# Kernel tuning notes

Hardware: AMD Instinct MI355X
Metric: run time of the kernel (lower is better)

## Reference

```python
import jax, jax.numpy as jnp
import numpy as np

B, L, E, H = 4, 1024, 2048, 16
DH = E // H
SCALE_BASE = 512.0


def _rotate_every_two(x):
    x1 = x[..., ::2]
    x2 = x[..., 1::2]
    return jnp.stack([-x2, x1], axis=-1).reshape(x.shape)


def _xpos(x, downscale):
    # x: [BH, L, Dh]; non-incremental path => offset = 0
    length = x.shape[1]
    head_dim = x.shape[-1]
    min_pos = -(length // 2)
    positions = jnp.arange(min_pos, length + min_pos, dtype=jnp.float32)  # [L]
    base = (jnp.arange(0, head_dim, 2, dtype=jnp.float32) + 0.4 * head_dim) / (1.4 * head_dim)  # [Dh/2]
    scale = base[None, :] ** (positions[:, None] / SCALE_BASE)  # [L, Dh/2]
    # fixed_pos_embedding over `scale` (seq_len=L, dim=Dh/2), positions 0..L-1
    dim = head_dim // 2
    inv_freq = 1.0 / (10000.0 ** (jnp.arange(0, dim, dtype=jnp.float32) / dim))
    sinusoid = jnp.arange(length, dtype=jnp.float32)[:, None] * inv_freq[None, :]
    sin, cos = jnp.sin(sinusoid), jnp.cos(sinusoid)
    if downscale:
        scale = 1.0 / scale
    sin_s = jnp.repeat(sin * scale, 2, axis=-1)  # duplicate_interleave -> [L, Dh]
    cos_s = jnp.repeat(cos * scale, 2, axis=-1)
    return x * cos_s + _rotate_every_two(x) * sin_s


def setup_inputs() -> dict:
    key = jax.random.key(0)
    ks = jax.random.split(key, 6)
    w_std = 1.0 / np.sqrt(E)
    query = jax.random.normal(ks[0], (B, L, E), dtype=jnp.float32)
    Wq = jax.random.normal(ks[1], (E, E), dtype=jnp.float32) * w_std
    Wk = jax.random.normal(ks[2], (E, E), dtype=jnp.float32) * w_std
    Wv = jax.random.normal(ks[3], (E, E), dtype=jnp.float32) * w_std
    Wo = jax.random.normal(ks[4], (E, E), dtype=jnp.float32) * w_std
    bq = jnp.zeros((E,), jnp.float32)
    bk = jnp.zeros((E,), jnp.float32)
    bv = jnp.zeros((E,), jnp.float32)
    bo = jnp.zeros((E,), jnp.float32)
    # causal additive mask [L, L]: 0 on/below diag, large negative above
    attn_mask = jnp.where(jnp.triu(jnp.ones((L, L), bool), k=1), -1e9, 0.0).astype(jnp.float32)
    rel_pos = jax.random.normal(ks[5], (B * H, L, L), dtype=jnp.float32) * 0.02
    return {"query": query, "Wq": Wq, "bq": bq, "Wk": Wk, "bk": bk, "Wv": Wv,
            "bv": bv, "Wo": Wo, "bo": bo, "attn_mask": attn_mask, "rel_pos": rel_pos}


def reference(query, Wq, bq, Wk, bk, Wv, bv, Wo, bo, attn_mask, rel_pos):
    scaling = DH ** -0.5
    q = (query @ Wq.T + bq) * scaling
    k = query @ Wk.T + bk
    v = query @ Wv.T + bv

    def split(t):  # [B, L, E] -> [B*H, L, Dh]
        return t.reshape(B, L, H, DH).transpose(0, 2, 1, 3).reshape(B * H, L, DH)

    q, k, v = split(q), split(k), split(v)
    k = _xpos(k, downscale=True)
    q = _xpos(q, downscale=False)

    w = jnp.einsum('btd,bsd->bts', q, k)          # [B*H, L, L]
    w = jnp.nan_to_num(w) + attn_mask[None]
    w = w + rel_pos
    w = jax.nn.softmax(w.astype(jnp.float32), axis=-1).astype(w.dtype)
    attn = jnp.einsum('bts,bsd->btd', w, v)       # [B*H, L, Dh]
    attn = attn.reshape(B, H, L, DH).transpose(0, 2, 1, 3).reshape(B, L, E)
    out = attn @ Wo.T + bo
    attn_weights = w.reshape(B, H, L, L).transpose(1, 0, 2, 3)  # [H, B, L, L]
    return out, attn_weights
```

## Files before the change

kernel.cpp:

```cpp
#include <hip/hip_runtime.h>
#include <math.h>

#define BB 4
#define LL 1024
#define EE 2048
#define HH 16
#define DHD 128
#define NTOK 4096
#define NBH 64
#define OUT0_ELEMS 8388608

typedef __attribute__((ext_vector_type(8))) short short8;
typedef __attribute__((ext_vector_type(4))) float f32x4;
typedef __attribute__((ext_vector_type(4))) unsigned short ushort4v;
typedef __attribute__((ext_vector_type(8))) unsigned short ushort8v;

__device__ __forceinline__ unsigned short f2bf(float x) {
    union { float f; unsigned int u; } v; v.f = x;
    unsigned int r = v.u + 0x7FFFu + ((v.u >> 16) & 1u);
    return (unsigned short)(r >> 16);
}
__device__ __forceinline__ float bf2f(unsigned short h) {
    union { unsigned int u; float f; } v; v.u = ((unsigned int)h) << 16;
    return v.f;
}

__device__ __forceinline__ void gload16(const void* g, void* l) {
    __builtin_amdgcn_global_load_lds((const __attribute__((address_space(1))) void*)g,
                                     (__attribute__((address_space(3))) void*)l,
                                     16, 0, 0);
}

__global__ __launch_bounds__(256) void cvt_k(const float* __restrict__ in,
                                             unsigned short* __restrict__ out, int n) {
    int i = (blockIdx.x * 256 + threadIdx.x) * 8;
    if (i >= n) return;
    float4 a = *(const float4*)(in + i);
    float4 b = *(const float4*)(in + i + 4);
    ushort4v u, w;
    u.x = f2bf(a.x); u.y = f2bf(a.y); u.z = f2bf(a.z); u.w = f2bf(a.w);
    w.x = f2bf(b.x); w.y = f2bf(b.y); w.z = f2bf(b.z); w.w = f2bf(b.w);
    *(ushort4v*)(out + i) = u;
    *(ushort4v*)(out + i + 4) = w;
}

__global__ __launch_bounds__(64) void xpos_table_k(float4* __restrict__ tab) {
    int t = blockIdx.x;
    int j = threadIdx.x;
    float pos = (float)(t - 512);
    float base = (2.0f * (float)j + 51.2f) * (1.0f / 179.2f);
    float sc = powf(base, pos * (1.0f / 512.0f));
    float inv_freq = powf(10000.0f, -(float)j * (1.0f / 64.0f));
    float ang = (float)t * inv_freq;
    float s = sinf(ang);
    float c = cosf(ang);
    tab[(t << 6) | j] = make_float4(c * sc, s * sc, c / sc, s / sc);
}

__global__ __launch_bounds__(256) void xpos_apply_k(unsigned short* __restrict__ q,
                                                    unsigned short* __restrict__ k,
                                                    const float4* __restrict__ tab) {
    int g = blockIdx.x * 256 + threadIdx.x;
    int jj = g & 15;
    int t = (g >> 4) & 1023;
    int bh = g >> 14;
    size_t off = (((size_t)((bh << 10) | t)) << 7) + jj * 8;
    ushort8v qv = *(const ushort8v*)(q + off);
    ushort8v kv = *(const ushort8v*)(k + off);
    ushort8v qo, ko;
#pragma unroll
    for (int p = 0; p < 4; ++p) {
        float4 tb = tab[(t << 6) | (jj * 4 + p)];
        float qx = bf2f(qv[2 * p]), qy = bf2f(qv[2 * p + 1]);
        float kx = bf2f(kv[2 * p]), ky = bf2f(kv[2 * p + 1]);
        qo[2 * p]     = f2bf(qx * tb.x - qy * tb.y);
        qo[2 * p + 1] = f2bf(qy * tb.x + qx * tb.y);
        ko[2 * p]     = f2bf(kx * tb.z - ky * tb.w);
        ko[2 * p + 1] = f2bf(ky * tb.z + kx * tb.w);
    }
    *(ushort8v*)(q + off) = qo;
    *(ushort8v*)(k + off) = ko;
}

__global__ __launch_bounds__(256)
void mmqkv_k(const unsigned short* __restrict__ Abf, const unsigned short* __restrict__ Wqkv,
             const float* __restrict__ bq, const float* __restrict__ bk,
             const float* __restrict__ bv, unsigned short* __restrict__ qb,
             unsigned short* __restrict__ kb, unsigned short* __restrict__ vt,
             float scaling) {
    __shared__ alignas(16) unsigned short lA[128 * 32];
    __shared__ alignas(16) unsigned short lB[128 * 32];

    const int tid = threadIdx.x;
    const int lane = tid & 63;
    const int wave = tid >> 6;
    const int wr = wave >> 1, wc = wave & 1;
    const int fr = lane & 15, fq = lane >> 4;
    const int m0 = blockIdx.y * 128, n0 = blockIdx.x * 128;
    const int w = n0 >> 11;
    const float* bsel = (w == 0) ? bq : (w == 1) ? bk : bv;
    const float alpha = (w == 0) ? scaling : 1.0f;

    f32x4 acc[4][4];
#pragma unroll
    for (int i = 0; i < 4; ++i)
#pragma unroll
        for (int j = 0; j < 4; ++j) acc[i][j] = (f32x4){0.f, 0.f, 0.f, 0.f};

    for (int k0 = 0; k0 < 2048; k0 += 32) {
#pragma unroll
        for (int i = 0; i < 2; ++i) {
            int c = i * 256 + tid;
            int r = c >> 2, kc = c & 3;
            gload16(Abf + (size_t)(m0 + r) * 2048 + k0 + kc * 8, &lA[c * 8]);
        }
#pragma unroll
        for (int i = 0; i < 2; ++i) {
            int c = i * 256 + tid;
            int r = c >> 2, kc = c & 3;
            gload16(Wqkv + (size_t)(n0 + r) * 2048 + k0 + kc * 8, &lB[c * 8]);
        }
        __syncthreads();

        short8 afr[4], bfr[4];
#pragma unroll
        for (int mi = 0; mi < 4; ++mi)
            afr[mi] = *(const short8*)&lA[(wr * 64 + mi * 16 + fr) * 32 + fq * 8];
#pragma unroll
        for (int ni = 0; ni < 4; ++ni)
            bfr[ni] = *(const short8*)&lB[(wc * 64 + ni * 16 + fr) * 32 + fq * 8];
#pragma unroll
        for (int mi = 0; mi < 4; ++mi)
#pragma unroll
            for (int ni = 0; ni < 4; ++ni)
                acc[mi][ni] = __builtin_amdgcn_mfma_f32_16x16x32_bf16(
                    afr[mi], bfr[ni], acc[mi][ni], 0, 0, 0);
        __syncthreads();
    }

#pragma unroll
    for (int mi = 0; mi < 4; ++mi) {
#pragma unroll
        for (int ni = 0; ni < 4; ++ni) {
#pragma unroll
            for (int r = 0; r < 4; ++r) {
                int m = m0 + wr * 64 + mi * 16 + fq * 4 + r;
                int n = n0 + wc * 64 + ni * 16 + fr;
                int nn = n & 2047;
                int b_ = m >> 10, t = m & 1023, h = nn >> 7, d = nn & 127;
                float v = alpha * (acc[mi][ni][r] + bsel[nn]);
                if (w == 0)
                    qb[(((size_t)(b_ * HH + h) << 10 | t) << 7) | d] = f2bf(v);
                else if (w == 1)
                    kb[(((size_t)(b_ * HH + h) << 10 | t) << 7) | d] = f2bf(v);
                else
                    vt[((size_t)((b_ * HH + h) * 128 + d) << 10) | t] = f2bf(v);
            }
        }
    }
}

__global__ __launch_bounds__(256)
void mmo_k(const unsigned short* __restrict__ Abf, const unsigned short* __restrict__ Bp,
           const float* __restrict__ bias, float* __restrict__ C) {
    __shared__ alignas(16) unsigned short lA[128 * 32];
    __shared__ alignas(16) unsigned short lB[128 * 32];

    const int tid = threadIdx.x;
    const int lane = tid & 63;
    const int wave = tid >> 6;
    const int wr = wave >> 1, wc = wave & 1;
    const int fr = lane & 15, fq = lane >> 4;
    const int m0 = blockIdx.y * 128, n0 = blockIdx.x * 128;

    f32x4 acc[4][4];
#pragma unroll
    for (int i = 0; i < 4; ++i)
#pragma unroll
        for (int j = 0; j < 4; ++j) acc[i][j] = (f32x4){0.f, 0.f, 0.f, 0.f};

    for (int k0 = 0; k0 < 2048; k0 += 32) {
#pragma unroll
        for (int i = 0; i < 2; ++i) {
            int c = i * 256 + tid;
            int r = c >> 2, kc = c & 3;
            gload16(Abf + (size_t)(m0 + r) * 2048 + k0 + kc * 8, &lA[c * 8]);
        }
#pragma unroll
        for (int i = 0; i < 2; ++i) {
            int c = i * 256 + tid;
            int r = c >> 2, kc = c & 3;
            gload16(Bp + (size_t)(n0 + r) * 2048 + k0 + kc * 8, &lB[c * 8]);
        }
        __syncthreads();

        short8 afr[4], bfr[4];
#pragma unroll
        for (int mi = 0; mi < 4; ++mi)
            afr[mi] = *(const short8*)&lA[(wr * 64 + mi * 16 + fr) * 32 + fq * 8];
#pragma unroll
        for (int ni = 0; ni < 4; ++ni)
            bfr[ni] = *(const short8*)&lB[(wc * 64 + ni * 16 + fr) * 32 + fq * 8];
#pragma unroll
        for (int mi = 0; mi < 4; ++mi)
#pragma unroll
            for (int ni = 0; ni < 4; ++ni)
                acc[mi][ni] = __builtin_amdgcn_mfma_f32_16x16x32_bf16(
                    afr[mi], bfr[ni], acc[mi][ni], 0, 0, 0);
        __syncthreads();
    }

#pragma unroll
    for (int mi = 0; mi < 4; ++mi)
#pragma unroll
        for (int ni = 0; ni < 4; ++ni)
#pragma unroll
            for (int r = 0; r < 4; ++r) {
                int m = m0 + wr * 64 + mi * 16 + fq * 4 + r;
                int n = n0 + wc * 64 + ni * 16 + fr;
                C[(size_t)m * EE + n] = acc[mi][ni][r] + bias[n];
            }
}

__global__ __launch_bounds__(256)
void scores_k(const unsigned short* __restrict__ qb, const unsigned short* __restrict__ kb,
              const float* __restrict__ rel, unsigned short* __restrict__ ebuf,
              float* __restrict__ psum) {
    __shared__ alignas(16) char smem[16384];
    unsigned short* lA = (unsigned short*)smem;
    unsigned short* lB = (unsigned short*)(smem + 8192);
    float* slab = (float*)smem;

    const int tid = threadIdx.x;
    const int lane = tid & 63, wave = tid >> 6;
    const int wr = wave >> 1, wc = wave & 1;
    const int fr = lane & 15, fq = lane >> 4;

    int idx = blockIdx.x;
    int tt = (int)((sqrtf(8.f * (float)idx + 1.f) - 1.f) * 0.5f);
    while ((tt + 1) * (tt + 2) / 2 <= idx) ++tt;
    while (tt * (tt + 1) / 2 > idx) --tt;
    const int ss = idx - tt * (tt + 1) / 2;
    const int t0 = tt << 7, s0 = ss << 7;
    const int bh = blockIdx.y;

    const unsigned short* Q = qb + ((size_t)bh << 17);
    const unsigned short* K = kb + ((size_t)bh << 17);

    f32x4 acc[4][4];
#pragma unroll
    for (int i = 0; i < 4; ++i)
#pragma unroll
        for (int j = 0; j < 4; ++j) acc[i][j] = (f32x4){0.f, 0.f, 0.f, 0.f};

    for (int k0 = 0; k0 < 128; k0 += 32) {
#pragma unroll
        for (int i = 0; i < 2; ++i) {
            int c = i * 256 + tid;
            int r = c >> 2, kc = c & 3;
            gload16(Q + (size_t)(t0 + r) * 128 + k0 + kc * 8, &lA[c * 8]);
        }
#pragma unroll
        for (int i = 0; i < 2; ++i) {
            int c = i * 256 + tid;
            int r = c >> 2, kc = c & 3;
            gload16(K + (size_t)(s0 + r) * 128 + k0 + kc * 8, &lB[c * 8]);
        }
        __syncthreads();

        short8 afr[4], bfr[4];
#pragma unroll
        for (int mi = 0; mi < 4; ++mi)
            afr[mi] = *(const short8*)&lA[(wr * 64 + mi * 16 + fr) * 32 + fq * 8];
#pragma unroll
        for (int ni = 0; ni < 4; ++ni)
            bfr[ni] = *(const short8*)&lB[(wc * 64 + ni * 16 + fr) * 32 + fq * 8];
#pragma unroll
        for (int mi = 0; mi < 4; ++mi)
#pragma unroll
            for (int ni = 0; ni < 4; ++ni)
                acc[mi][ni] = __builtin_amdgcn_mfma_f32_16x16x32_bf16(
                    afr[mi], bfr[ni], acc[mi][ni], 0, 0, 0);
        __syncthreads();
    }

    unsigned short* EO = ebuf + ((size_t)bh << 20);
    const float* RLb = rel + ((size_t)bh << 20);
#pragma unroll
    for (int sl = 0; sl < 4; ++sl) {
        if (wr == (sl >> 1)) {
#pragma unroll
            for (int mi2 = 0; mi2 < 2; ++mi2) {
                int mi = ((sl & 1) << 1) + mi2;
#pragma unroll
                for (int ni = 0; ni < 4; ++ni)
#pragma unroll
                    for (int r = 0; r < 4; ++r) {
                        int srow = (mi2 << 4) + (fq << 2) + r;
                        int col = (wc << 6) + (ni << 4) + fr;
                        slab[srow * 128 + (col ^ (((srow >> 2) & 3) << 4))] = acc[mi][ni][r];
                    }
            }
        }
        __syncthreads();
        {
            int srow = tid >> 3;
            int tg = t0 + (sl << 5) + srow;
            const float* RL = RLb + ((size_t)tg << 10) + s0;
            unsigned short* ER = EO + ((size_t)tg << 10) + s0;
            float rsum = 0.f;
#pragma unroll
            for (int c = 0; c < 4; ++c) {
                int col = ((tid & 7) << 2) + (c << 5);
                float4 sv = *(const float4*)&slab[srow * 128 + (col ^ (((srow >> 2) & 3) << 4))];
                float4 rl = *(const float4*)(RL + col);
                float4 e;
                e.x = (s0 + col     <= tg) ? __expf(sv.x + rl.x - 15.f) : 0.f;
                e.y = (s0 + col + 1 <= tg) ? __expf(sv.y + rl.y - 15.f) : 0.f;
                e.z = (s0 + col + 2 <= tg) ? __expf(sv.z + rl.z - 15.f) : 0.f;
                e.w = (s0 + col + 3 <= tg) ? __expf(sv.w + rl.w - 15.f) : 0.f;
                ushort4v h;
                h.x = f2bf(e.x); h.y = f2bf(e.y); h.z = f2bf(e.z); h.w = f2bf(e.w);
                *(ushort4v*)(ER + col) = h;
                rsum += e.x + e.y + e.z + e.w;
            }
            rsum += __shfl_xor(rsum, 1);
            rsum += __shfl_xor(rsum, 2);
            rsum += __shfl_xor(rsum, 4);
            if ((tid & 7) == 0)
                psum[((((size_t)bh << 10) + tg) << 3) + ss] = rsum;
        }
        __syncthreads();
    }
}

__global__ __launch_bounds__(256)
void pvw_k(const unsigned short* __restrict__ ebuf, const unsigned short* __restrict__ vt,
           const float* __restrict__ psum, float* __restrict__ attnP,
           unsigned short* __restrict__ am) {
    __shared__ alignas(16) unsigned short lE[64 * 64];
    __shared__ alignas(16) unsigned short lV[128 * 64];
    __shared__ float lInvF[64];

    const int tid = threadIdx.x;
    const int lane = tid & 63, wave = tid >> 6;
    const int wr = wave >> 1, wc = wave & 1;
    const int fr = lane & 15, fq = lane >> 4;
    const int strip = 15 - blockIdx.x;
    const int t0 = strip << 6;
    const int bh = blockIdx.y;
    const int hh = bh & 15, bb = bh >> 4;
    const int n_s = (t0 >> 6) + 1;

    const unsigned short* EB = ebuf + ((size_t)bh << 20) + ((size_t)t0 << 10);
    const unsigned short* Vb = vt + ((size_t)bh << 17);
    float* PO = attnP + (((size_t)(hh * BB + bb)) << 20) + ((size_t)t0 << 10);

    if (tid < 64) {
        const float* p = psum + ((((size_t)bh << 10) + t0 + tid) << 3);
        const int tt = t0 >> 7;
        float s = 0.f;
#pragma unroll
        for (int j = 0; j < 8; ++j) s += (j <= tt) ? p[j] : 0.f;
        lInvF[tid] = 1.f / s;
    }
    __syncthreads();

    f32x4 acc[2][4];
#pragma unroll
    for (int i = 0; i < 2; ++i)
#pragma unroll
        for (int j = 0; j < 4; ++j) acc[i][j] = (f32x4){0.f, 0.f, 0.f, 0.f};

    for (int j = 0; j < n_s; ++j) {
        int s0 = j << 6;
#pragma unroll
        for (int i = 0; i < 2; ++i) {
            int o = (i * 256 + tid) * 16;
            int r = o >> 7;
            int cb = (o & 127) ^ ((r & 7) << 4);
            gload16(EB + (size_t)r * 1024 + s0 + (cb >> 1), (char*)lE + o);
        }
#pragma unroll
        for (int i = 0; i < 4; ++i) {
            int o = (i * 256 + tid) * 16;
            int r = o >> 7;
            int cb = (o & 127) ^ ((r & 7) << 4);
            gload16(Vb + (size_t)r * 1024 + s0 + (cb >> 1), (char*)lV + o);
        }
        __syncthreads();

        {
            int row = tid >> 2, col0 = (tid & 3) << 4;
            float inv = lInvF[row];
            float* PR = PO + (size_t)row * 1024 + s0 + col0;
#pragma unroll
            for (int cc = 0; cc < 2; ++cc) {
                int cbyte = ((col0 + cc * 8) * 2) ^ ((row & 7) << 4);
                ushort8v ev = *(const ushort8v*)((const char*)lE + row * 128 + cbyte);
                float4 p0, p1;
                p0.x = bf2f(ev[0]) * inv; p0.y = bf2f(ev[1]) * inv;
                p0.z = bf2f(ev[2]) * inv; p0.w = bf2f(ev[3]) * inv;
                p1.x = bf2f(ev[4]) * inv; p1.y = bf2f(ev[5]) * inv;
                p1.z = bf2f(ev[6]) * inv; p1.w = bf2f(ev[7]) * inv;
                *(float4*)(PR + cc * 8) = p0;
                *(float4*)(PR + cc * 8 + 4) = p1;
            }
        }

#pragma unroll
        for (int ks = 0; ks < 2; ++ks) {
            short8 pf[2], vf[4];
#pragma unroll
            for (int mi = 0; mi < 2; ++mi) {
                int row = wr * 32 + mi * 16 + fr;
                int cb = (ks * 64 + fq * 16) ^ ((row & 7) << 4);
                pf[mi] = *(const short8*)((const char*)lE + row * 128 + cb);
            }
#pragma unroll
            for (int ni = 0; ni < 4; ++ni) {
                int row = wc * 64 + ni * 16 + fr;
                int cb = (ks * 64 + fq * 16) ^ ((row & 7) << 4);
                vf[ni] = *(const short8*)((const char*)lV + row * 128 + cb);
            }
#pragma unroll
            for (int mi = 0; mi < 2; ++mi)
#pragma unroll
                for (int ni = 0; ni < 4; ++ni)
                    acc[mi][ni] = __builtin_amdgcn_mfma_f32_16x16x32_bf16(
                        pf[mi], vf[ni], acc[mi][ni], 0, 0, 0);
        }
        __syncthreads();
    }

    {
        int row = tid >> 2;
        float4 z = make_float4(0.f, 0.f, 0.f, 0.f);
        for (int c = (n_s << 6) + ((tid & 3) << 2); c < 1024; c += 16)
            *(float4*)(PO + (size_t)row * 1024 + c) = z;
    }

#pragma unroll
    for (int mi = 0; mi < 2; ++mi)
#pragma unroll
        for (int ni = 0; ni < 4; ++ni)
#pragma unroll
            for (int r = 0; r < 4; ++r) {
                int tl = wr * 32 + mi * 16 + fq * 4 + r;
                int d = wc * 64 + ni * 16 + fr;
                float o = acc[mi][ni][r] * lInvF[tl];
                am[(((size_t)(bb * 1024 + t0 + tl)) << 11) + hh * 128 + d] = f2bf(o);
            }
}

extern "C" void kernel_launch(void* const* d_in, const int* in_sizes, int n_in,
                              void* d_out, int out_size, void* d_ws, size_t ws_size,
                              hipStream_t stream) {
    const float* query = (const float*)d_in[0];
    const float* Wq    = (const float*)d_in[1];
    const float* bq    = (const float*)d_in[2];
    const float* Wk    = (const float*)d_in[3];
    const float* bk    = (const float*)d_in[4];
    const float* Wv    = (const float*)d_in[5];
    const float* bv    = (const float*)d_in[6];
    const float* Wo    = (const float*)d_in[7];
    const float* bo    = (const float*)d_in[8];
    const float* rel   = (const float*)d_in[10];

    float* out    = (float*)d_out;
    float* attn_w = out + OUT0_ELEMS;

    char* w = (char*)d_ws;
    unsigned short* Xbf   = (unsigned short*)(w);
    unsigned short* Wqkvb = (unsigned short*)(w + (16 << 20));
    unsigned short* Wob   = (unsigned short*)(w + (40 << 20));
    unsigned short* qb    = (unsigned short*)(w + (48 << 20));
    unsigned short* kb    = (unsigned short*)(w + (64 << 20));
    unsigned short* vt    = (unsigned short*)(w + (80 << 20));
    unsigned short* am    = (unsigned short*)(w + (96 << 20));
    float4* tab           = (float4*)(w + (112 << 20));
    float* psum           = (float*)(w + (113u << 20));
    unsigned short* ebuf  = (unsigned short*)(w + (128u << 20));

    const float scaling = 0.08838834764831845f;

    xpos_table_k<<<LL, 64, 0, stream>>>(tab);

    cvt_k<<<4096, 256, 0, stream>>>(query, Xbf, OUT0_ELEMS);
    cvt_k<<<2048, 256, 0, stream>>>(Wq, Wqkvb, EE * EE);
    cvt_k<<<2048, 256, 0, stream>>>(Wk, Wqkvb + (size_t)EE * EE, EE * EE);
    cvt_k<<<2048, 256, 0, stream>>>(Wv, Wqkvb + 2 * (size_t)EE * EE, EE * EE);
    cvt_k<<<2048, 256, 0, stream>>>(Wo, Wob, EE * EE);

    dim3 gqkv(3 * EE / 128, NTOK / 128);
    mmqkv_k<<<gqkv, 256, 0, stream>>>(Xbf, Wqkvb, bq, bk, bv, qb, kb, vt, scaling);

    xpos_apply_k<<<(NBH * LL * 16) / 256, 256, 0, stream>>>(qb, kb, tab);

    dim3 gsc(36, NBH);
    scores_k<<<gsc, 256, 0, stream>>>(qb, kb, rel, ebuf, psum);

    dim3 gpv(16, NBH);
    pvw_k<<<gpv, 256, 0, stream>>>(ebuf, vt, psum, attn_w, am);

    dim3 gout(EE / 128, NTOK / 128);
    mmo_k<<<gout, 256, 0, stream>>>(am, Wob, bo, out);
}
```

Measured before the change: 481.5 us.

## Fuse weight conversions, fold xPos into QKV epilogue, reorder PV grid

The five fp32-to-bf16 conversion launches are merged into one kernel that indexes into the right source and destination. The xPos rotation is moved into the QKV GEMM epilogue: each lane gets its partner element with a lane shuffle and reads the sin/cos table, which removes the separate read-modify-write pass over q and k. The PV kernel grid is transposed so that blocks for heavy causal strips across all heads are scheduled first. The trade-off is extra table loads and shuffles in the GEMM epilogue.

After: 472.0 us. -2.0%, faster.

```diff
diff --git a/kernel.cpp b/kernel.cpp
--- a/kernel.cpp
+++ b/kernel.cpp
@@ -31,17 +31,31 @@
                                      16, 0, 0);
 }
 
-__global__ __launch_bounds__(256) void cvt_k(const float* __restrict__ in,
-                                             unsigned short* __restrict__ out, int n) {
-    int i = (blockIdx.x * 256 + threadIdx.x) * 8;
-    if (i >= n) return;
-    float4 a = *(const float4*)(in + i);
-    float4 b = *(const float4*)(in + i + 4);
+__global__ __launch_bounds__(256)
+void cvt_all_k(const float* __restrict__ X, const float* __restrict__ Wq,
+               const float* __restrict__ Wk, const float* __restrict__ Wv,
+               const float* __restrict__ Wo, unsigned short* __restrict__ Xbf,
+               unsigned short* __restrict__ Wqkvb, unsigned short* __restrict__ Wob) {
+    size_t g = (size_t)(blockIdx.x * 256 + threadIdx.x) * 8;
+    if (g >= 25165824u) return;
+    const float* src;
+    unsigned short* dst;
+    if (g < 8388608u) {
+        src = X + g; dst = Xbf + g;
+    } else {
+        size_t rr = g - 8388608u;
+        int wi = (int)(rr >> 22);
+        size_t o = rr & 4194303u;
+        src = (wi == 0 ? Wq : wi == 1 ? Wk : wi == 2 ? Wv : Wo) + o;
+        dst = (wi < 3 ? Wqkvb + ((size_t)wi << 22) : Wob) + o;
+    }
+    float4 a = *(const float4*)(src);
+    float4 b = *(const float4*)(src + 4);
     ushort4v u, w;
     u.x = f2bf(a.x); u.y = f2bf(a.y); u.z = f2bf(a.z); u.w = f2bf(a.w);
     w.x = f2bf(b.x); w.y = f2bf(b.y); w.z = f2bf(b.z); w.w = f2bf(b.w);
-    *(ushort4v*)(out + i) = u;
-    *(ushort4v*)(out + i + 4) = w;
+    *(ushort4v*)(dst) = u;
+    *(ushort4v*)(dst + 4) = w;
 }
 
 __global__ __launch_bounds__(64) void xpos_table_k(float4* __restrict__ tab) {
@@ -57,37 +71,12 @@
     tab[(t << 6) | j] = make_float4(c * sc, s * sc, c / sc, s / sc);
 }
 
-__global__ __launch_bounds__(256) void xpos_apply_k(unsigned short* __restrict__ q,
-                                                    unsigned short* __restrict__ k,
-                                                    const float4* __restrict__ tab) {
-    int g = blockIdx.x * 256 + threadIdx.x;
-    int jj = g & 15;
-    int t = (g >> 4) & 1023;
-    int bh = g >> 14;
-    size_t off = (((size_t)((bh << 10) | t)) << 7) + jj * 8;
-    ushort8v qv = *(const ushort8v*)(q + off);
-    ushort8v kv = *(const ushort8v*)(k + off);
-    ushort8v qo, ko;
-#pragma unroll
-    for (int p = 0; p < 4; ++p) {
-        float4 tb = tab[(t << 6) | (jj * 4 + p)];
-        float qx = bf2f(qv[2 * p]), qy = bf2f(qv[2 * p + 1]);
-        float kx = bf2f(kv[2 * p]), ky = bf2f(kv[2 * p + 1]);
-        qo[2 * p]     = f2bf(qx * tb.x - qy * tb.y);
-        qo[2 * p + 1] = f2bf(qy * tb.x + qx * tb.y);
-        ko[2 * p]     = f2bf(kx * tb.z - ky * tb.w);
-        ko[2 * p + 1] = f2bf(ky * tb.z + kx * tb.w);
-    }
-    *(ushort8v*)(q + off) = qo;
-    *(ushort8v*)(k + off) = ko;
-}
-
 __global__ __launch_bounds__(256)
 void mmqkv_k(const unsigned short* __restrict__ Abf, const unsigned short* __restrict__ Wqkv,
              const float* __restrict__ bq, const float* __restrict__ bk,
              const float* __restrict__ bv, unsigned short* __restrict__ qb,
              unsigned short* __restrict__ kb, unsigned short* __restrict__ vt,
-             float scaling) {
+             const float4* __restrict__ tab, float scaling) {
     __shared__ alignas(16) unsigned short lA[128 * 32];
     __shared__ alignas(16) unsigned short lB[128 * 32];
 
@@ -142,19 +131,26 @@
     for (int mi = 0; mi < 4; ++mi) {
 #pragma unroll
         for (int ni = 0; ni < 4; ++ni) {
+            int n = n0 + wc * 64 + ni * 16 + fr;
+            int nn = n & 2047;
+            int h = nn >> 7, d = nn & 127;
+            float bias = bsel[nn];
 #pragma unroll
             for (int r = 0; r < 4; ++r) {
                 int m = m0 + wr * 64 + mi * 16 + fq * 4 + r;
-                int n = n0 + wc * 64 + ni * 16 + fr;
-                int nn = n & 2047;
-                int b_ = m >> 10, t = m & 1023, h = nn >> 7, d = nn & 127;
-                float v = alpha * (acc[mi][ni][r] + bsel[nn]);
-                if (w == 0)
-                    qb[(((size_t)(b_ * HH + h) << 10 | t) << 7) | d] = f2bf(v);
-                else if (w == 1)
-                    kb[(((size_t)(b_ * HH + h) << 10 | t) << 7) | d] = f2bf(v);
-                else
+                int b_ = m >> 10, t = m & 1023;
+                float v = alpha * (acc[mi][ni][r] + bias);
+                if (w < 2) {
+                    float pv = __shfl_xor(v, 1);
+                    float4 tb = tab[(t << 6) | (d >> 1)];
+                    float c = (w == 0) ? tb.x : tb.z;
+                    float s = (w == 0) ? tb.y : tb.w;
+                    float rot = (d & 1) ? (v * c + pv * s) : (v * c - pv * s);
+                    unsigned short* dst = (w == 0) ? qb : kb;
+                    dst[(((size_t)(b_ * HH + h) << 10 | t) << 7) | d] = f2bf(rot);
+                } else {
                     vt[((size_t)((b_ * HH + h) * 128 + d) << 10) | t] = f2bf(v);
+                }
             }
         }
     }
@@ -346,9 +342,9 @@
     const int lane = tid & 63, wave = tid >> 6;
     const int wr = wave >> 1, wc = wave & 1;
     const int fr = lane & 15, fq = lane >> 4;
-    const int strip = 15 - blockIdx.x;
+    const int strip = 15 - blockIdx.y;
     const int t0 = strip << 6;
-    const int bh = blockIdx.y;
+    const int bh = blockIdx.x;
     const int hh = bh & 15, bb = bh >> 4;
     const int n_s = (t0 >> 6) + 1;
 
@@ -486,21 +482,15 @@
 
     xpos_table_k<<<LL, 64, 0, stream>>>(tab);
 
-    cvt_k<<<4096, 256, 0, stream>>>(query, Xbf, OUT0_ELEMS);
-    cvt_k<<<2048, 256, 0, stream>>>(Wq, Wqkvb, EE * EE);
-    cvt_k<<<2048, 256, 0, stream>>>(Wk, Wqkvb + (size_t)EE * EE, EE * EE);
-    cvt_k<<<2048, 256, 0, stream>>>(Wv, Wqkvb + 2 * (size_t)EE * EE, EE * EE);
-    cvt_k<<<2048, 256, 0, stream>>>(Wo, Wob, EE * EE);
+    cvt_all_k<<<12288, 256, 0, stream>>>(query, Wq, Wk, Wv, Wo, Xbf, Wqkvb, Wob);
 
     dim3 gqkv(3 * EE / 128, NTOK / 128);
-    mmqkv_k<<<gqkv, 256, 0, stream>>>(Xbf, Wqkvb, bq, bk, bv, qb, kb, vt, scaling);
-
-    xpos_apply_k<<<(NBH * LL * 16) / 256, 256, 0, stream>>>(qb, kb, tab);
+    mmqkv_k<<<gqkv, 256, 0, stream>>>(Xbf, Wqkvb, bq, bk, bv, qb, kb, vt, tab, scaling);
 
     dim3 gsc(36, NBH);
     scores_k<<<gsc, 256, 0, stream>>>(qb, kb, rel, ebuf, psum);
 
-    dim3 gpv(16, NBH);
+    dim3 gpv(NBH, 16);
     pvw_k<<<gpv, 256, 0, stream>>>(ebuf, vt, psum, attn_w, am);
 
     dim3 gout(EE / 128, NTOK / 128);
```
